# Kernel optimization log

Hardware: AMD Instinct MI355X
Metric: run time of the kernel (lower is better)

Reference implementation:

```python
import jax, jax.numpy as jnp
import numpy as np

N_EMBED = 1024
HEAD_SIZE = 128

def setup_inputs() -> dict:
    key = jax.random.key(0)
    k1, k2, k3, k4 = jax.random.split(key, 4)
    x = jax.random.normal(k1, (8, 2048, N_EMBED), dtype=jnp.float32)
    # torch.nn.Linear default init: U(-1/sqrt(in), 1/sqrt(in)); stored as [out, in],
    # we store transposed [in, out] for x @ W.
    bound = 1.0 / np.sqrt(N_EMBED)
    Wk = jax.random.uniform(k2, (N_EMBED, HEAD_SIZE), jnp.float32, -bound, bound)
    Wq = jax.random.uniform(k3, (N_EMBED, HEAD_SIZE), jnp.float32, -bound, bound)
    Wv = jax.random.uniform(k4, (N_EMBED, HEAD_SIZE), jnp.float32, -bound, bound)
    return {"x": x, "Wk": Wk, "Wq": Wq, "Wv": Wv}

def reference(x, Wk, Wq, Wv):
    # x: [B, T, E]
    k = jnp.einsum('bte,eh->bth', x, Wk)  # [B, T, H]
    q = jnp.einsum('bte,eh->bth', x, Wq)
    v = jnp.einsum('bte,eh->bth', x, Wv)
    scale = 1.0 / np.sqrt(HEAD_SIZE).astype(np.float32)
    wei = jnp.einsum('bqh,bkh->bqk', q, k) * scale  # [B, T, T]
    wei = jax.nn.softmax(wei, axis=-1)
    out = jnp.einsum('bqk,bkh->bqh', wei, v)  # [B, T, H]
    return out
```

## Files before the change

### kernel.cpp

```cpp
#include <hip/hip_runtime.h>

#define BATCH 8
#define TLEN 2048
#define EMB 1024
#define HDIM 128
#define SCALE 0.08838834764831845f
#define NSPLIT 4

typedef _Float16 f16x8 __attribute__((ext_vector_type(8)));
typedef _Float16 f16x4 __attribute__((ext_vector_type(4)));
typedef float f32x4 __attribute__((ext_vector_type(4)));

static __device__ __forceinline__ f32x4 mfma16(f16x8 a, f16x8 b, f32x4 c) {
    return __builtin_amdgcn_mfma_f32_16x16x32_f16(a, b, c, 0, 0, 0);
}

__global__ void prep_w(const float* __restrict__ Wk, const float* __restrict__ Wq,
                       const float* __restrict__ Wv, _Float16* __restrict__ wt) {
    int i = blockIdx.x * 256 + threadIdx.x;
    int w = i >> 17;
    int r = i & 131071;
    int h = r >> 10;
    int k = r & 1023;
    const float* src = (w == 0) ? Wk : (w == 1) ? Wq : Wv;
    float v = src[k * HDIM + h];
    if (w == 1) v *= SCALE;
    wt[i] = (_Float16)v;
}

__global__ __launch_bounds__(256, 2) void proj_kernel(
        const float* __restrict__ x, const _Float16* __restrict__ wt,
        _Float16* __restrict__ kb, _Float16* __restrict__ qb, _Float16* __restrict__ vbT) {
    __shared__ _Float16 xs[32 * 72];
    __shared__ _Float16 wsb[384 * 68];
    const int t = threadIdx.x;
    const int m0 = blockIdx.x * 32;
    const int wv = t >> 6;
    const int lane = t & 63;
    const int m16 = lane & 15;
    const int quad = lane >> 4;
    const int n0 = wv * 96;

    const f32x4 zero4 = {0.f, 0.f, 0.f, 0.f};
    f32x4 acc[2][6];
#pragma unroll
    for (int mt = 0; mt < 2; mt++)
#pragma unroll
        for (int nt = 0; nt < 6; nt++) acc[mt][nt] = zero4;

    for (int k0 = 0; k0 < EMB; k0 += 64) {
        __syncthreads();
#pragma unroll
        for (int i = 0; i < 12; i++) {
            int u = t + i * 256;
            int row = u >> 3, seg = u & 7;
            *(f16x8*)&wsb[row * 68 + seg * 8] =
                *(const f16x8*)&wt[(size_t)row * EMB + k0 + seg * 8];
        }
#pragma unroll
        for (int i = 0; i < 2; i++) {
            int u = t + i * 256;
            int row = u >> 4, col = (u & 15) * 4;
            float4 xv = *(const float4*)&x[(size_t)(m0 + row) * EMB + k0 + col];
            f16x4 h;
            h[0] = (_Float16)xv.x; h[1] = (_Float16)xv.y;
            h[2] = (_Float16)xv.z; h[3] = (_Float16)xv.w;
            *(f16x4*)&xs[row * 72 + col] = h;
        }
        __syncthreads();
#pragma unroll
        for (int ks = 0; ks < 2; ks++) {
            f16x8 af[2], bf[6];
#pragma unroll
            for (int mt = 0; mt < 2; mt++)
                af[mt] = *(const f16x8*)&xs[(mt * 16 + m16) * 72 + ks * 32 + quad * 8];
#pragma unroll
            for (int nt = 0; nt < 6; nt++)
                bf[nt] = *(const f16x8*)&wsb[(n0 + nt * 16 + m16) * 68 + ks * 32 + quad * 8];
#pragma unroll
            for (int mt = 0; mt < 2; mt++)
#pragma unroll
                for (int nt = 0; nt < 6; nt++)
                    acc[mt][nt] = mfma16(af[mt], bf[nt], acc[mt][nt]);
        }
    }
#pragma unroll
    for (int nt = 0; nt < 6; nt++) {
        int n = n0 + nt * 16 + m16;
        int nsel = n >> 7;
        int h = n & 127;
        if (nsel < 2) {
            _Float16* dst = (nsel == 0) ? kb : qb;
#pragma unroll
            for (int mt = 0; mt < 2; mt++)
#pragma unroll
                for (int r = 0; r < 4; r++) {
                    int mg = m0 + mt * 16 + quad * 4 + r;
                    dst[(size_t)mg * HDIM + h] = (_Float16)acc[mt][nt][r];
                }
        } else {
#pragma unroll
            for (int mt = 0; mt < 2; mt++) {
                int mg = m0 + mt * 16 + quad * 4;
                int bb = mg >> 11, tok = mg & 2047;
                f16x4 pk;
#pragma unroll
                for (int r = 0; r < 4; r++) pk[r] = (_Float16)acc[mt][nt][r];
                *(f16x4*)&vbT[((size_t)bb * HDIM + h) * TLEN + tok] = pk;
            }
        }
    }
}

__global__ __launch_bounds__(256, 2) void attn_kernel(
        const _Float16* __restrict__ qb, const _Float16* __restrict__ kb,
        const _Float16* __restrict__ vbT,
        float* __restrict__ po, float* __restrict__ pl) {
    __shared__ _Float16 kls[64 * 136];
    __shared__ _Float16 vtl[128 * 72];
    __shared__ _Float16 pls[4 * 32 * 72];
    const int t = threadIdx.x;
    const int qt = blockIdx.x;
    const int b = blockIdx.y;
    const int sp = blockIdx.z;
    const int wv = t >> 6;
    const int lane = t & 63;
    const int m16 = lane & 15;
    const int quad = lane >> 4;
    const int q0 = qt * 128 + wv * 32;
    _Float16* pw = pls + wv * (32 * 72);

    f16x8 qf[2][4];
#pragma unroll
    for (int mt = 0; mt < 2; mt++)
#pragma unroll
        for (int ks = 0; ks < 4; ks++)
            qf[mt][ks] = *(const f16x8*)
                &qb[((size_t)b * TLEN + q0 + mt * 16 + m16) * HDIM + ks * 32 + quad * 8];

    f16x8 ones;
#pragma unroll
    for (int j = 0; j < 8; j++) ones[j] = (_Float16)1.0f;

    const f32x4 zero4 = {0.f, 0.f, 0.f, 0.f};
    f32x4 o[2][8], ol[2];
#pragma unroll
    for (int mt = 0; mt < 2; mt++) {
        ol[mt] = zero4;
#pragma unroll
        for (int nt = 0; nt < 8; nt++) o[mt][nt] = zero4;
    }

    for (int kt = sp * 8; kt < sp * 8 + 8; kt++) {
        const int k0 = kt * 64;
        __syncthreads();
#pragma unroll
        for (int rep = 0; rep < 4; rep++) {
            int u = t + rep * 256;
            int i = u >> 4, seg = u & 15;
            *(f16x8*)&kls[i * 136 + seg * 8] =
                *(const f16x8*)&kb[((size_t)b * TLEN + k0 + i) * HDIM + seg * 8];
        }
#pragma unroll
        for (int rep = 0; rep < 4; rep++) {
            int u = t + rep * 256;
            int h = u >> 3, seg = u & 7;
            *(f16x8*)&vtl[h * 72 + seg * 8] =
                *(const f16x8*)&vbT[((size_t)b * HDIM + h) * TLEN + k0 + seg * 8];
        }
        __syncthreads();
        f32x4 s[2][4];
#pragma unroll
        for (int mt = 0; mt < 2; mt++)
#pragma unroll
            for (int nt = 0; nt < 4; nt++) s[mt][nt] = zero4;
#pragma unroll
        for (int nt = 0; nt < 4; nt++)
#pragma unroll
            for (int ks = 0; ks < 4; ks++) {
                f16x8 bf = *(const f16x8*)&kls[(nt * 16 + m16) * 136 + ks * 32 + quad * 8];
                s[0][nt] = mfma16(qf[0][ks], bf, s[0][nt]);
                s[1][nt] = mfma16(qf[1][ks], bf, s[1][nt]);
            }
#pragma unroll
        for (int mt = 0; mt < 2; mt++)
#pragma unroll
            for (int nt = 0; nt < 4; nt++)
#pragma unroll
                for (int r = 0; r < 4; r++)
                    pw[(mt * 16 + quad * 4 + r) * 72 + nt * 16 + m16] =
                        (_Float16)__expf(s[mt][nt][r]);
        f16x8 ap[2][2];
#pragma unroll
        for (int mt = 0; mt < 2; mt++)
#pragma unroll
            for (int h = 0; h < 2; h++)
                ap[mt][h] = *(const f16x8*)&pw[(mt * 16 + m16) * 72 + h * 32 + quad * 8];
#pragma unroll
        for (int mt = 0; mt < 2; mt++) {
            ol[mt] = mfma16(ap[mt][0], ones, ol[mt]);
            ol[mt] = mfma16(ap[mt][1], ones, ol[mt]);
        }
#pragma unroll
        for (int nt = 0; nt < 8; nt++) {
            f16x8 b0 = *(const f16x8*)&vtl[(nt * 16 + m16) * 72 + quad * 8];
            f16x8 b1 = *(const f16x8*)&vtl[(nt * 16 + m16) * 72 + 32 + quad * 8];
            o[0][nt] = mfma16(ap[0][0], b0, o[0][nt]);
            o[0][nt] = mfma16(ap[0][1], b1, o[0][nt]);
            o[1][nt] = mfma16(ap[1][0], b0, o[1][nt]);
            o[1][nt] = mfma16(ap[1][1], b1, o[1][nt]);
        }
    }
#pragma unroll
    for (int mt = 0; mt < 2; mt++)
#pragma unroll
        for (int r = 0; r < 4; r++) {
            int row = q0 + mt * 16 + quad * 4 + r;
            size_t prow = ((size_t)(sp * BATCH + b)) * TLEN + row;
#pragma unroll
            for (int nt = 0; nt < 8; nt++)
                po[prow * HDIM + nt * 16 + m16] = o[mt][nt][r];
            if (m16 == 0) pl[prow] = ol[mt][r];
        }
}

__global__ void combine_kernel(const float* __restrict__ po, const float* __restrict__ pl,
                               float* __restrict__ out) {
    int g = blockIdx.x * 256 + threadIdx.x;
    int row = g >> 5;
    int part = g & 31;
    int bb = row >> 11;
    int tok = row & 2047;
    float L = 0.f;
    float4 acc = {0.f, 0.f, 0.f, 0.f};
#pragma unroll
    for (int s = 0; s < NSPLIT; s++) {
        size_t prow = ((size_t)(s * BATCH + bb)) * TLEN + tok;
        L += pl[prow];
        float4 p = *(const float4*)&po[prow * HDIM + part * 4];
        acc.x += p.x; acc.y += p.y; acc.z += p.z; acc.w += p.w;
    }
    float inv = 1.f / L;
    float4 res = {acc.x * inv, acc.y * inv, acc.z * inv, acc.w * inv};
    *(float4*)&out[(size_t)row * HDIM + part * 4] = res;
}

extern "C" void kernel_launch(void* const* d_in, const int* in_sizes, int n_in,
                              void* d_out, int out_size, void* d_ws, size_t ws_size,
                              hipStream_t stream) {
    const float* x  = (const float*)d_in[0];
    const float* Wk = (const float*)d_in[1];
    const float* Wq = (const float*)d_in[2];
    const float* Wv = (const float*)d_in[3];
    float* out = (float*)d_out;
    char* ws = (char*)d_ws;
    _Float16* wt  = (_Float16*)(ws);
    _Float16* kb  = (_Float16*)(ws + (1ull << 20));
    _Float16* qb  = (_Float16*)(ws + (5ull << 20));
    _Float16* vbT = (_Float16*)(ws + (9ull << 20));
    float* po = (float*)(ws + (13ull << 20));
    float* pl = (float*)(ws + (13ull << 20) + 33554432ull);

    prep_w<<<dim3(1536), dim3(256), 0, stream>>>(Wk, Wq, Wv, wt);
    proj_kernel<<<dim3(512), dim3(256), 0, stream>>>(x, wt, kb, qb, vbT);
    attn_kernel<<<dim3(16, BATCH, NSPLIT), dim3(256), 0, stream>>>(qb, kb, vbT, po, pl);
    combine_kernel<<<dim3(2048), dim3(256), 0, stream>>>(po, pl, out);
}
```

Measured before the change: 160.5 us.

## Pre-swizzle weights into MFMA fragment order and prefetch tiles into registers

The weight prep kernel now writes W in the exact per-lane MFMA B-fragment order, so the projection kernel loads B fragments straight from global memory and no longer stages a 384-row weight tile in shared memory. The projection and attention kernels now issue global loads into registers before the barrier and write them to LDS afterwards, so memory latency can overlap the previous iteration. The QK^T product is transposed (K as the A operand) so each thread writes its exp'd scores to LDS as packed 4-wide vectors instead of scalar stores. This trades LDS traffic and occupancy for more register pressure and direct global fragment loads, which may not coalesce as well.

```diff
diff --git a/kernel.cpp b/kernel.cpp
--- a/kernel.cpp
+++ b/kernel.cpp
@@ -16,23 +16,30 @@
 }
 
 __global__ void prep_w(const float* __restrict__ Wk, const float* __restrict__ Wq,
-                       const float* __restrict__ Wv, _Float16* __restrict__ wt) {
-    int i = blockIdx.x * 256 + threadIdx.x;
-    int w = i >> 17;
-    int r = i & 131071;
-    int h = r >> 10;
-    int k = r & 1023;
-    const float* src = (w == 0) ? Wk : (w == 1) ? Wq : Wv;
-    float v = src[k * HDIM + h];
-    if (w == 1) v *= SCALE;
-    wt[i] = (_Float16)v;
+                       const float* __restrict__ Wv, _Float16* __restrict__ wtf) {
+    int g = blockIdx.x * 256 + threadIdx.x;
+    int lane = g & 63;
+    int kstep = (g >> 6) & 31;
+    int ntile = g >> 11;
+    int n = ntile * 16 + (lane & 15);
+    int sel = n >> 7;
+    int h = n & 127;
+    const float* W = (sel == 0) ? Wk : (sel == 1) ? Wq : Wv;
+    int kbase = kstep * 32 + (lane >> 4) * 8;
+    f16x8 o;
+#pragma unroll
+    for (int j = 0; j < 8; j++) {
+        float v = W[(size_t)(kbase + j) * HDIM + h];
+        if (sel == 1) v *= SCALE;
+        o[j] = (_Float16)v;
+    }
+    *(f16x8*)&wtf[(size_t)g * 8] = o;
 }
 
 __global__ __launch_bounds__(256, 2) void proj_kernel(
-        const float* __restrict__ x, const _Float16* __restrict__ wt,
+        const float* __restrict__ x, const _Float16* __restrict__ wtf,
         _Float16* __restrict__ kb, _Float16* __restrict__ qb, _Float16* __restrict__ vbT) {
     __shared__ _Float16 xs[32 * 72];
-    __shared__ _Float16 wsb[384 * 68];
     const int t = threadIdx.x;
     const int m0 = blockIdx.x * 32;
     const int wv = t >> 6;
@@ -49,39 +56,44 @@
         for (int nt = 0; nt < 6; nt++) acc[mt][nt] = zero4;
 
     for (int k0 = 0; k0 < EMB; k0 += 64) {
-        __syncthreads();
-#pragma unroll
-        for (int i = 0; i < 12; i++) {
-            int u = t + i * 256;
-            int row = u >> 3, seg = u & 7;
-            *(f16x8*)&wsb[row * 68 + seg * 8] =
-                *(const f16x8*)&wt[(size_t)row * EMB + k0 + seg * 8];
-        }
+        f16x8 bf[2][6];
+#pragma unroll
+        for (int ks = 0; ks < 2; ks++) {
+            int kstep = (k0 >> 5) + ks;
+#pragma unroll
+            for (int nt = 0; nt < 6; nt++) {
+                int ntile = wv * 6 + nt;
+                bf[ks][nt] = *(const f16x8*)
+                    &wtf[(size_t)((ntile * 32 + kstep) * 64 + lane) * 8];
+            }
+        }
+        float4 xv[2];
 #pragma unroll
         for (int i = 0; i < 2; i++) {
             int u = t + i * 256;
-            int row = u >> 4, col = (u & 15) * 4;
-            float4 xv = *(const float4*)&x[(size_t)(m0 + row) * EMB + k0 + col];
+            xv[i] = *(const float4*)&x[(size_t)(m0 + (u >> 4)) * EMB + k0 + (u & 15) * 4];
+        }
+        __syncthreads();
+#pragma unroll
+        for (int i = 0; i < 2; i++) {
+            int u = t + i * 256;
             f16x4 h;
-            h[0] = (_Float16)xv.x; h[1] = (_Float16)xv.y;
-            h[2] = (_Float16)xv.z; h[3] = (_Float16)xv.w;
-            *(f16x4*)&xs[row * 72 + col] = h;
+            h[0] = (_Float16)xv[i].x; h[1] = (_Float16)xv[i].y;
+            h[2] = (_Float16)xv[i].z; h[3] = (_Float16)xv[i].w;
+            *(f16x4*)&xs[(u >> 4) * 72 + (u & 15) * 4] = h;
         }
         __syncthreads();
 #pragma unroll
         for (int ks = 0; ks < 2; ks++) {
-            f16x8 af[2], bf[6];
+            f16x8 af[2];
 #pragma unroll
             for (int mt = 0; mt < 2; mt++)
                 af[mt] = *(const f16x8*)&xs[(mt * 16 + m16) * 72 + ks * 32 + quad * 8];
 #pragma unroll
-            for (int nt = 0; nt < 6; nt++)
-                bf[nt] = *(const f16x8*)&wsb[(n0 + nt * 16 + m16) * 68 + ks * 32 + quad * 8];
-#pragma unroll
             for (int mt = 0; mt < 2; mt++)
 #pragma unroll
                 for (int nt = 0; nt < 6; nt++)
-                    acc[mt][nt] = mfma16(af[mt], bf[nt], acc[mt][nt]);
+                    acc[mt][nt] = mfma16(af[mt], bf[ks][nt], acc[mt][nt]);
         }
     }
 #pragma unroll
@@ -153,49 +165,50 @@
 
     for (int kt = sp * 8; kt < sp * 8 + 8; kt++) {
         const int k0 = kt * 64;
-        __syncthreads();
+        f16x8 kreg[4], vreg[4];
 #pragma unroll
         for (int rep = 0; rep < 4; rep++) {
             int u = t + rep * 256;
-            int i = u >> 4, seg = u & 15;
-            *(f16x8*)&kls[i * 136 + seg * 8] =
-                *(const f16x8*)&kb[((size_t)b * TLEN + k0 + i) * HDIM + seg * 8];
-        }
+            kreg[rep] = *(const f16x8*)
+                &kb[((size_t)b * TLEN + k0 + (u >> 4)) * HDIM + (u & 15) * 8];
+            vreg[rep] = *(const f16x8*)
+                &vbT[((size_t)b * HDIM + (u >> 3)) * TLEN + k0 + (u & 7) * 8];
+        }
+        __syncthreads();
 #pragma unroll
         for (int rep = 0; rep < 4; rep++) {
             int u = t + rep * 256;
-            int h = u >> 3, seg = u & 7;
-            *(f16x8*)&vtl[h * 72 + seg * 8] =
-                *(const f16x8*)&vbT[((size_t)b * HDIM + h) * TLEN + k0 + seg * 8];
-        }
-        __syncthreads();
-        f32x4 s[2][4];
+            *(f16x8*)&kls[(u >> 4) * 136 + (u & 15) * 8] = kreg[rep];
+            *(f16x8*)&vtl[(u >> 3) * 72 + (u & 7) * 8] = vreg[rep];
+        }
+        __syncthreads();
+        f32x4 st[4][2];
+#pragma unroll
+        for (int kt_ = 0; kt_ < 4; kt_++) {
+            st[kt_][0] = zero4; st[kt_][1] = zero4;
+#pragma unroll
+            for (int ks = 0; ks < 4; ks++) {
+                f16x8 kf = *(const f16x8*)&kls[(kt_ * 16 + m16) * 136 + ks * 32 + quad * 8];
+                st[kt_][0] = mfma16(kf, qf[0][ks], st[kt_][0]);
+                st[kt_][1] = mfma16(kf, qf[1][ks], st[kt_][1]);
+            }
+        }
+#pragma unroll
+        for (int kt_ = 0; kt_ < 4; kt_++)
+#pragma unroll
+            for (int mt = 0; mt < 2; mt++) {
+                f16x4 pk;
+#pragma unroll
+                for (int r = 0; r < 4; r++)
+                    pk[r] = (_Float16)__expf(st[kt_][mt][r]);
+                *(f16x4*)&pw[(mt * 16 + m16) * 72 + kt_ * 16 + quad * 4] = pk;
+            }
+        f16x8 ap[2][2];
 #pragma unroll
         for (int mt = 0; mt < 2; mt++)
 #pragma unroll
-            for (int nt = 0; nt < 4; nt++) s[mt][nt] = zero4;
-#pragma unroll
-        for (int nt = 0; nt < 4; nt++)
-#pragma unroll
-            for (int ks = 0; ks < 4; ks++) {
-                f16x8 bf = *(const f16x8*)&kls[(nt * 16 + m16) * 136 + ks * 32 + quad * 8];
-                s[0][nt] = mfma16(qf[0][ks], bf, s[0][nt]);
-                s[1][nt] = mfma16(qf[1][ks], bf, s[1][nt]);
-            }
-#pragma unroll
-        for (int mt = 0; mt < 2; mt++)
-#pragma unroll
-            for (int nt = 0; nt < 4; nt++)
-#pragma unroll
-                for (int r = 0; r < 4; r++)
-                    pw[(mt * 16 + quad * 4 + r) * 72 + nt * 16 + m16] =
-                        (_Float16)__expf(s[mt][nt][r]);
-        f16x8 ap[2][2];
-#pragma unroll
-        for (int mt = 0; mt < 2; mt++)
-#pragma unroll
-            for (int h = 0; h < 2; h++)
-                ap[mt][h] = *(const f16x8*)&pw[(mt * 16 + m16) * 72 + h * 32 + quad * 8];
+            for (int kc = 0; kc < 2; kc++)
+                ap[mt][kc] = *(const f16x8*)&pw[(mt * 16 + m16) * 72 + kc * 32 + quad * 8];
 #pragma unroll
         for (int mt = 0; mt < 2; mt++) {
             ol[mt] = mfma16(ap[mt][0], ones, ol[mt]);
@@ -254,15 +267,15 @@
     const float* Wv = (const float*)d_in[3];
     float* out = (float*)d_out;
     char* ws = (char*)d_ws;
-    _Float16* wt  = (_Float16*)(ws);
+    _Float16* wtf = (_Float16*)(ws);
     _Float16* kb  = (_Float16*)(ws + (1ull << 20));
     _Float16* qb  = (_Float16*)(ws + (5ull << 20));
     _Float16* vbT = (_Float16*)(ws + (9ull << 20));
     float* po = (float*)(ws + (13ull << 20));
     float* pl = (float*)(ws + (13ull << 20) + 33554432ull);
 
-    prep_w<<<dim3(1536), dim3(256), 0, stream>>>(Wk, Wq, Wv, wt);
-    proj_kernel<<<dim3(512), dim3(256), 0, stream>>>(x, wt, kb, qb, vbT);
+    prep_w<<<dim3(192), dim3(256), 0, stream>>>(Wk, Wq, Wv, wtf);
+    proj_kernel<<<dim3(512), dim3(256), 0, stream>>>(x, wtf, kb, qb, vbT);
     attn_kernel<<<dim3(16, BATCH, NSPLIT), dim3(256), 0, stream>>>(qb, kb, vbT, po, pl);
     combine_kernel<<<dim3(2048), dim3(256), 0, stream>>>(po, pl, out);
 }
```

Result: no change. 157.9 us (-1.6%).
